# Performance work log

Hardware: AMD Instinct MI355X
Metric: run time of the kernel (lower is better)

Reference implementation:

```python
import jax, jax.numpy as jnp
import numpy as np
import math

NUM_HEADS = 8
EMBED = 512
D_K = EMBED // NUM_HEADS
B, T1, T2 = 16, 512, 512
N_POS = 2 * T1 - 1


def rel_shift(x, left_context=0):
    # x: (B, H, T1, 2*T1-1) -> (B, H, T1, T2), out[i, j] = x[i, j - i + T1 - 1]
    t1 = x.shape[2]
    t2 = t1 + left_context
    idx = jnp.arange(t2)[None, :] - jnp.arange(t1)[:, None] + (t1 - 1)  # (T1, T2)
    return jnp.take_along_axis(x, idx[None, None, :, :], axis=-1)


def setup_inputs() -> dict:
    key = jax.random.key(0)
    ks = jax.random.split(key, 16)
    scale = 1.0 / math.sqrt(EMBED)
    inp = {
        "query": jax.random.normal(ks[0], (B, T1, EMBED), jnp.float32),
        "key": jax.random.normal(ks[1], (B, T2, EMBED), jnp.float32),
        "value": jax.random.normal(ks[2], (B, T2, EMBED), jnp.float32),
        "pos_enc": jax.random.normal(ks[3], (B, N_POS, EMBED), jnp.float32),
        "mask": jnp.zeros((B, T2), dtype=bool),
        "chunk_mask": jnp.zeros((T1, T1), dtype=bool),
        "Wq": jax.random.normal(ks[4], (EMBED, EMBED), jnp.float32) * scale,
        "bq": jnp.zeros((EMBED,), jnp.float32),
        "Wk": jax.random.normal(ks[5], (EMBED, EMBED), jnp.float32) * scale,
        "bk": jnp.zeros((EMBED,), jnp.float32),
        "Wv": jax.random.normal(ks[6], (EMBED, EMBED), jnp.float32) * scale,
        "bv": jnp.zeros((EMBED,), jnp.float32),
        "Wpos": jax.random.normal(ks[7], (EMBED, EMBED), jnp.float32) * scale,
        "Wo": jax.random.normal(ks[8], (EMBED, EMBED), jnp.float32) * scale,
        "bo": jnp.zeros((EMBED,), jnp.float32),
        "pos_bias_u": jax.random.normal(ks[9], (NUM_HEADS, D_K), jnp.float32) * 0.1,
        "pos_bias_v": jax.random.normal(ks[10], (NUM_HEADS, D_K), jnp.float32) * 0.1,
        "left_context": 0,
    }
    return inp


def reference(query, key, value, pos_enc, mask, chunk_mask, Wq, bq, Wk, bk, Wv, bv,
              Wpos, Wo, bo, pos_bias_u, pos_bias_v, left_context):
    b, t1, _ = query.shape
    t2 = key.shape[1]
    # qkv projections -> (B, T, H, d_k)
    q = (query @ Wq.T + bq).reshape(b, t1, NUM_HEADS, D_K)
    k = (key @ Wk.T + bk).reshape(b, t2, NUM_HEADS, D_K)
    v = (value @ Wv.T + bv).reshape(b, t2, NUM_HEADS, D_K)
    # positional projection (no bias) -> (B, N, H, d_k)
    p = (pos_enc @ Wpos.T).reshape(b, -1, NUM_HEADS, D_K)
    # content and positional scores
    matrix_ac = jnp.einsum('bihd,bjhd->bhij', q + pos_bias_u, k)  # (B,H,T1,T2)
    matrix_bd = jnp.einsum('bihd,bnhd->bhin', q + pos_bias_v, p)  # (B,H,T1,N)
    matrix_bd = rel_shift(matrix_bd, left_context=left_context)   # (B,H,T1,T2)
    scores = (matrix_ac + matrix_bd) / math.sqrt(D_K)
    # combined mask: True = masked
    m = chunk_mask[None, None, :, :] | mask[:, None, None, :]
    neg_inf = jnp.finfo(scores.dtype).min
    scores = jnp.where(m, neg_inf, scores)
    attn = jax.nn.softmax(scores, axis=-1)
    attn = jnp.where(m, 0.0, attn)
    out = jnp.einsum('bhij,bjhd->bihd', attn, v).reshape(b, t1, NUM_HEADS * D_K)
    return out @ Wo.T + bo
```

## Files before the change

kernel.cpp:

```cpp
#include <hip/hip_runtime.h>
#include <math.h>

typedef _Float16 f16;
typedef f16 f16x8 __attribute__((ext_vector_type(8)));
typedef f16 f16x4 __attribute__((ext_vector_type(4)));
typedef float f32x4 __attribute__((ext_vector_type(4)));

#define H_   8
#define E_   512
#define DK   64
#define NPOS 1023

#define GLL(SRC, DST) __builtin_amdgcn_global_load_lds( \
    (const __attribute__((address_space(1))) void*)(SRC), \
    (__attribute__((address_space(3))) void*)(DST), 16, 0, 0)

struct CSeg { const float* src; f16* dst; int n4; };
struct CArgs { CSeg s[9]; };
__global__ __launch_bounds__(256) void conv_f16(CArgs a) {
    const int stride = gridDim.x * 256;
    const int gid = blockIdx.x * 256 + threadIdx.x;
    for (int si = 0; si < 9; ++si) {
        const float* __restrict__ src = a.s[si].src;
        f16* __restrict__ dst = a.s[si].dst;
        const int n4 = a.s[si].n4;
        for (int i = gid; i < n4; i += stride) {
            const float4 v = ((const float4*)src)[i];
            f16x4 h; h[0] = (f16)v.x; h[1] = (f16)v.y; h[2] = (f16)v.z; h[3] = (f16)v.w;
            ((f16x4*)dst)[i] = h;
        }
    }
}

struct PArg {
    const f16* A; const f16* W; const float* bias; const float* bias2;
    void* C; int Mvalid; int mode;
};
struct PArgs { PArg g[4]; };

__device__ __forceinline__ void gemm128_body(const PArg g, int bx, int by) {
    __shared__ __align__(16) f16 Al[128 * 32];
    __shared__ __align__(16) f16 Wl[128 * 32];
    const int tid = threadIdx.x;
    const int lane = tid & 63, w = tid >> 6;
    const int quad = lane >> 4, l15 = lane & 15;
    const int wr = w >> 1, wc = w & 1;
    const int m0 = by * 128, n0 = bx * 128;

    const int r0 = w * 32 + (lane >> 2);
    const int c0 = (lane & 3) * 8;
    int ar0 = m0 + r0;      if (ar0 >= g.Mvalid) ar0 = g.Mvalid - 1;
    int ar1 = m0 + r0 + 16; if (ar1 >= g.Mvalid) ar1 = g.Mvalid - 1;
    const f16* A0 = g.A + (size_t)ar0 * 512 + c0;
    const f16* A1 = g.A + (size_t)ar1 * 512 + c0;
    const f16* W0 = g.W + (size_t)(n0 + r0) * 512 + c0;
    const f16* W1 = g.W + (size_t)(n0 + r0 + 16) * 512 + c0;
    f16* const lA0 = &Al[(w * 32) * 32];
    f16* const lA1 = &Al[(w * 32 + 16) * 32];
    f16* const lW0 = &Wl[(w * 32) * 32];
    f16* const lW1 = &Wl[(w * 32 + 16) * 32];

    f32x4 acc[4][4];
    #pragma unroll
    for (int m = 0; m < 4; ++m)
        #pragma unroll
        for (int n = 0; n < 4; ++n) acc[m][n] = (f32x4){0.f, 0.f, 0.f, 0.f};

    for (int ki = 0; ki < 16; ++ki) {
        const int k0 = ki * 32;
        if (ki) __syncthreads();
        GLL(A0 + k0, lA0);
        GLL(A1 + k0, lA1);
        GLL(W0 + k0, lW0);
        GLL(W1 + k0, lW1);
        __syncthreads();

        f16x8 af[4], bf[4];
        #pragma unroll
        for (int m = 0; m < 4; ++m)
            af[m] = *(const f16x8*)&Al[(wr * 64 + m * 16 + l15) * 32 + quad * 8];
        #pragma unroll
        for (int n = 0; n < 4; ++n)
            bf[n] = *(const f16x8*)&Wl[(wc * 64 + n * 16 + l15) * 32 + quad * 8];
        #pragma unroll
        for (int m = 0; m < 4; ++m)
            #pragma unroll
            for (int n = 0; n < 4; ++n)
                acc[m][n] = __builtin_amdgcn_mfma_f32_16x16x32_f16(af[m], bf[n], acc[m][n], 0, 0, 0);
    }

    const int mq = m0 + wr * 64 + quad * 4;
    const int nq = n0 + wc * 64 + l15;
    #pragma unroll
    for (int m = 0; m < 4; ++m) {
        #pragma unroll
        for (int n = 0; n < 4; ++n) {
            const int gr0 = mq + m * 16;
            const int col = nq + n * 16;
            float bs = g.bias ? g.bias[col] : 0.f;
            if (g.bias2) bs += g.bias2[col];
            const f32x4 a = acc[m][n];
            if (g.mode == 0) {
                float* C = (float*)g.C;
                #pragma unroll
                for (int r = 0; r < 4; ++r) C[(size_t)(gr0 + r) * 512 + col] = a[r] + bs;
            } else if (g.mode == 1) {
                f16* C = (f16*)g.C;
                const int b = gr0 >> 9, t = gr0 & 511;
                const int hh = col >> 6, dk = col & 63;
                f16x4 hv;
                #pragma unroll
                for (int r = 0; r < 4; ++r) hv[r] = (f16)(a[r] + bs);
                *(f16x4*)&C[(((size_t)b * H_ + hh) * DK + dk) * 512 + t] = hv;
            } else if (g.mode == 2) {
                f16* C = (f16*)g.C;
                const int b = gr0 >> 9, t = gr0 & 511;
                const int hh = col >> 6, dk = col & 63;
                #pragma unroll
                for (int r = 0; r < 4; ++r)
                    C[(((size_t)b * H_ + hh) * 512 + t + r) * DK + dk] = (f16)(a[r] + bs);
            } else {
                f16* C = (f16*)g.C;
                const int hh = col >> 6, dk = col & 63;
                #pragma unroll
                for (int r = 0; r < 4; ++r) {
                    const int gm = gr0 + r;
                    if (gm < g.Mvalid) {
                        const int b = gm / NPOS, t = gm - b * NPOS;
                        C[(((size_t)b * H_ + hh) * NPOS + t) * DK + dk] = (f16)a[r];
                    }
                }
            }
        }
    }
}

__global__ __launch_bounds__(256, 4) void proj_all(PArgs a) {
    const int id = blockIdx.x;
    int gi, rem, nwg;
    if (id < 768) { gi = id >> 8; rem = id & 255; nwg = 256; }
    else          { gi = 3;       rem = id - 768; nwg = 512; }
    const int t = (rem & 7) * (nwg >> 3) + (rem >> 3);
    gemm128_body(a.g[gi], t & 3, t >> 2);
}
__global__ __launch_bounds__(256, 4) void proj_one(PArg g) {
    const int t = (blockIdx.x & 7) * 32 + (blockIdx.x >> 3);
    gemm128_body(g, t & 3, t >> 2);
}

__global__ __launch_bounds__(256) void attn_mfma(
    const f16* __restrict__ Qh,
    const f16* __restrict__ Kh,
    const f16* __restrict__ Vt,
    const f16* __restrict__ Ph,
    const float* __restrict__ pbu, const float* __restrict__ pbv,
    const unsigned char* __restrict__ bmask,
    const unsigned char* __restrict__ cmask,
    f16* __restrict__ CTX)
{
    __shared__ f16 Qa[64 * 72];
    __shared__ f16 Ka[64 * 72];
    __shared__ f16 Va[64 * 72];
    __shared__ f16 Pa[128 * 72];
    __shared__ unsigned char Ma[64 * 64];

    const int tid = threadIdx.x;
    const int lane = tid & 63, w = tid >> 6;
    const int quad = lane >> 4, l15 = lane & 15;
    const int id = blockIdx.x;
    const int lg = (id & 7) * 128 + (id >> 3);
    const int it = lg & 7, bh = lg >> 3;
    const int h = bh & 7, b = bh >> 3;
    const int i0 = it * 64;
    const int rowt = w * 16 + quad * 4;
    const int sr = tid >> 3, sc = (tid & 7) * 8;
    const int mr = tid >> 2, mc = (tid & 3) * 16;

    *(uint4*)&Qa[sr * 72 + sc] = *(const uint4*)&Qh[((size_t)bh * 512 + i0 + sr) * 64 + sc];
    *(uint4*)&Qa[(sr + 32) * 72 + sc] =
        *(const uint4*)&Qh[((size_t)bh * 512 + i0 + sr + 32) * 64 + sc];
    f16x8 dpbf[2];
    #pragma unroll
    for (int ks = 0; ks < 2; ++ks)
        #pragma unroll
        for (int j = 0; j < 8; ++j) {
            const int d = ks * 32 + quad * 8 + j;
            dpbf[ks][j] = (f16)(pbv[h * 64 + d] - pbu[h * 64 + d]);
        }

    float m_run[4], l_run[4];
    f32x4 accO[4];
    #pragma unroll
    for (int x = 0; x < 4; ++x) {
        m_run[x] = -__builtin_inff(); l_run[x] = 0.f;
        accO[x] = (f32x4){0.f, 0.f, 0.f, 0.f};
    }

    uint4 pK0, pK1, pV0, pV1, pP0, pP1, pP2, pP3, pM;
    {
        const int j0 = 0, nbase = 448 - i0;
        pK0 = *(const uint4*)&Kh[((size_t)bh * 512 + j0 + sr) * 64 + sc];
        pK1 = *(const uint4*)&Kh[((size_t)bh * 512 + j0 + sr + 32) * 64 + sc];
        pV0 = *(const uint4*)&Vt[((size_t)bh * 64 + sr) * 512 + j0 + sc];
        pV1 = *(const uint4*)&Vt[((size_t)bh * 64 + sr + 32) * 512 + j0 + sc];
        int n0_ = nbase + sr;       if (n0_ > NPOS - 1) n0_ = NPOS - 1;
        int n1_ = nbase + sr + 32;  if (n1_ > NPOS - 1) n1_ = NPOS - 1;
        int n2_ = nbase + sr + 64;  if (n2_ > NPOS - 1) n2_ = NPOS - 1;
        int n3_ = nbase + sr + 96;  if (n3_ > NPOS - 1) n3_ = NPOS - 1;
        pP0 = *(const uint4*)&Ph[((size_t)bh * NPOS + n0_) * 64 + sc];
        pP1 = *(const uint4*)&Ph[((size_t)bh * NPOS + n1_) * 64 + sc];
        pP2 = *(const uint4*)&Ph[((size_t)bh * NPOS + n2_) * 64 + sc];
        pP3 = *(const uint4*)&Ph[((size_t)bh * NPOS + n3_) * 64 + sc];
        const uint4 cm = *(const uint4*)&cmask[(size_t)(i0 + mr) * 512 + j0 + mc];
        const uint4 bm = *(const uint4*)&bmask[(size_t)b * 512 + j0 + mc];
        pM.x = cm.x | bm.x; pM.y = cm.y | bm.y; pM.z = cm.z | bm.z; pM.w = cm.w | bm.w;
    }

    for (int jt = 0; jt < 8; ++jt) {
        __syncthreads();
        *(uint4*)&Ka[sr * 72 + sc] = pK0;
        *(uint4*)&Ka[(sr + 32) * 72 + sc] = pK1;
        *(uint4*)&Va[sr * 72 + sc] = pV0;
        *(uint4*)&Va[(sr + 32) * 72 + sc] = pV1;
        *(uint4*)&Pa[sr * 72 + sc] = pP0;
        *(uint4*)&Pa[(sr + 32) * 72 + sc] = pP1;
        *(uint4*)&Pa[(sr + 64) * 72 + sc] = pP2;
        *(uint4*)&Pa[(sr + 96) * 72 + sc] = pP3;
        *(uint4*)&Ma[mr * 64 + mc] = pM;
        __syncthreads();

        if (jt < 7) {
            const int j0n = (jt + 1) * 64;
            const int nbase = j0n - i0 + 448;
            pK0 = *(const uint4*)&Kh[((size_t)bh * 512 + j0n + sr) * 64 + sc];
            pK1 = *(const uint4*)&Kh[((size_t)bh * 512 + j0n + sr + 32) * 64 + sc];
            pV0 = *(const uint4*)&Vt[((size_t)bh * 64 + sr) * 512 + j0n + sc];
            pV1 = *(const uint4*)&Vt[((size_t)bh * 64 + sr + 32) * 512 + j0n + sc];
            int n0_ = nbase + sr;       if (n0_ > NPOS - 1) n0_ = NPOS - 1;
            int n1_ = nbase + sr + 32;  if (n1_ > NPOS - 1) n1_ = NPOS - 1;
            int n2_ = nbase + sr + 64;  if (n2_ > NPOS - 1) n2_ = NPOS - 1;
            int n3_ = nbase + sr + 96;  if (n3_ > NPOS - 1) n3_ = NPOS - 1;
            pP0 = *(const uint4*)&Ph[((size_t)bh * NPOS + n0_) * 64 + sc];
            pP1 = *(const uint4*)&Ph[((size_t)bh * NPOS + n1_) * 64 + sc];
            pP2 = *(const uint4*)&Ph[((size_t)bh * NPOS + n2_) * 64 + sc];
            pP3 = *(const uint4*)&Ph[((size_t)bh * NPOS + n3_) * 64 + sc];
            const uint4 cm = *(const uint4*)&cmask[(size_t)(i0 + mr) * 512 + j0n + mc];
            const uint4 bm = *(const uint4*)&bmask[(size_t)b * 512 + j0n + mc];
            pM.x = cm.x | bm.x; pM.y = cm.y | bm.y; pM.z = cm.z | bm.z; pM.w = cm.w | bm.w;
        }

        f16x8 afQ[2], afV[2];
        #pragma unroll
        for (int ks = 0; ks < 2; ++ks) {
            afQ[ks] = *(const f16x8*)&Qa[(w * 16 + l15) * 72 + ks * 32 + quad * 8];
            afV[ks] = afQ[ks] + dpbf[ks];
        }
        f32x4 accAC[4];
        #pragma unroll
        for (int nt = 0; nt < 4; ++nt) {
            accAC[nt] = (f32x4){0.f, 0.f, 0.f, 0.f};
            #pragma unroll
            for (int ks = 0; ks < 2; ++ks) {
                const f16x8 bf = *(const f16x8*)&Ka[(nt * 16 + l15) * 72 + ks * 32 + quad * 8];
                accAC[nt] = __builtin_amdgcn_mfma_f32_16x16x32_f16(afQ[ks], bf, accAC[nt], 0, 0, 0);
            }
        }
        f32x4 accBD[5];
        #pragma unroll
        for (int u = 0; u < 5; ++u) {
            accBD[u] = (f32x4){0.f, 0.f, 0.f, 0.f};
            const int nts = (3 - w) + u;
            #pragma unroll
            for (int ks = 0; ks < 2; ++ks) {
                const f16x8 bf = *(const f16x8*)&Pa[(nts * 16 + l15) * 72 + ks * 32 + quad * 8];
                accBD[u] = __builtin_amdgcn_mfma_f32_16x16x32_f16(afV[ks], bf, accBD[u], 0, 0, 0);
            }
        }
        __syncthreads();

        #pragma unroll
        for (int rg = 0; rg < 4; ++rg) {
            const int qr = quad * 4 + rg;
            const int rt = rowt + rg;
            float tmpv[5];
            #pragma unroll
            for (int u = 0; u < 5; ++u) {
                const int cl = l15 + (3 + u) * 16 + qr - 63;
                const int dst = (quad * 16 + (cl & 15)) << 2;
                tmpv[u] = __uint_as_float(
                    (unsigned)__builtin_amdgcn_ds_permute(dst, (int)__float_as_uint(accBD[u][rg])));
            }
            const bool hi = l15 > qr;
            float sv[4]; unsigned mk = 0;
            #pragma unroll
            for (int nt = 0; nt < 4; ++nt) {
                const int c = nt * 16 + l15;
                const float bdv = hi ? tmpv[nt + 1] : tmpv[nt];
                float s = (accAC[nt][rg] + bdv) * 0.125f;
                if (Ma[rt * 64 + c]) { s = -3.402823466e38f; mk |= 1u << nt; }
                sv[nt] = s;
            }
            float tmax = fmaxf(fmaxf(sv[0], sv[1]), fmaxf(sv[2], sv[3]));
            #pragma unroll
            for (int d = 1; d < 16; d <<= 1) tmax = fmaxf(tmax, __shfl_xor(tmax, d));
            const float mnew = fmaxf(m_run[rg], tmax);
            const float alpha = __expf(m_run[rg] - mnew);
            float rsum = 0.f;
            f16 wv[4];
            #pragma unroll
            for (int nt = 0; nt < 4; ++nt) {
                const float e = __expf(sv[nt] - mnew);
                rsum += e;
                wv[nt] = ((mk >> nt) & 1u) ? (f16)0.f : (f16)e;
            }
            #pragma unroll
            for (int d = 1; d < 16; d <<= 1) rsum += __shfl_xor(rsum, d);
            l_run[rg] = l_run[rg] * alpha + rsum;
            m_run[rg] = mnew;
            #pragma unroll
            for (int dt = 0; dt < 4; ++dt) accO[dt][rg] *= alpha;
            #pragma unroll
            for (int nt = 0; nt < 4; ++nt)
                Ka[rt * 72 + nt * 16 + l15] = wv[nt];
        }
        f16x8 afW[2];
        #pragma unroll
        for (int ks = 0; ks < 2; ++ks)
            afW[ks] = *(const f16x8*)&Ka[(w * 16 + l15) * 72 + ks * 32 + quad * 8];
        #pragma unroll
        for (int dt = 0; dt < 4; ++dt)
            #pragma unroll
            for (int ks = 0; ks < 2; ++ks) {
                const f16x8 bf = *(const f16x8*)&Va[(dt * 16 + l15) * 72 + ks * 32 + quad * 8];
                accO[dt] = __builtin_amdgcn_mfma_f32_16x16x32_f16(afW[ks], bf, accO[dt], 0, 0, 0);
            }
    }

    #pragma unroll
    for (int rg = 0; rg < 4; ++rg) {
        const float inv = 1.0f / l_run[rg];
        const int gi = i0 + rowt + rg;
        #pragma unroll
        for (int dt = 0; dt < 4; ++dt)
            CTX[((size_t)b * 512 + gi) * 512 + h * 64 + dt * 16 + l15] = (f16)(accO[dt][rg] * inv);
    }
}

extern "C" void kernel_launch(void* const* d_in, const int* in_sizes, int n_in,
                              void* d_out, int out_size, void* d_ws, size_t ws_size,
                              hipStream_t stream) {
    const float* query   = (const float*)d_in[0];
    const float* key     = (const float*)d_in[1];
    const float* value   = (const float*)d_in[2];
    const float* pos_enc = (const float*)d_in[3];
    const unsigned char* mask       = (const unsigned char*)d_in[4];
    const unsigned char* chunk_mask = (const unsigned char*)d_in[5];
    const float* Wq  = (const float*)d_in[6];
    const float* bq  = (const float*)d_in[7];
    const float* Wk  = (const float*)d_in[8];
    const float* bk  = (const float*)d_in[9];
    const float* Wv  = (const float*)d_in[10];
    const float* bv  = (const float*)d_in[11];
    const float* Wpos = (const float*)d_in[12];
    const float* Wo   = (const float*)d_in[13];
    const float* bo   = (const float*)d_in[14];
    const float* pbu  = (const float*)d_in[15];
    const float* pbv  = (const float*)d_in[16];
    float* out = (float*)d_out;

    f16* base = (f16*)d_ws;
    size_t off = 0;
    f16* ctx  = base + off; off += 4194304;
    f16* Qhm  = base + off; off += 4194304;
    f16* Khm  = base + off; off += 4194304;
    f16* Vtm  = base + off; off += 4194304;
    f16* Phm  = base + off; off += 8380416;
    f16* qf   = base + off; off += 4194304;
    f16* kf   = base + off; off += 4194304;
    f16* vf   = base + off; off += 4194304;
    f16* pf   = base + off; off += 8380416;
    f16* wqf  = base + off; off += 262144;
    f16* wkf  = base + off; off += 262144;
    f16* wvf  = base + off; off += 262144;
    f16* wpf  = base + off; off += 262144;
    f16* wof  = base + off; off += 262144;

    CArgs ca;
    ca.s[0] = CSeg{pos_enc, pf,  2095104};
    ca.s[1] = CSeg{query,   qf,  1048576};
    ca.s[2] = CSeg{key,     kf,  1048576};
    ca.s[3] = CSeg{value,   vf,  1048576};
    ca.s[4] = CSeg{Wq,      wqf, 65536};
    ca.s[5] = CSeg{Wk,      wkf, 65536};
    ca.s[6] = CSeg{Wv,      wvf, 65536};
    ca.s[7] = CSeg{Wpos,    wpf, 65536};
    ca.s[8] = CSeg{Wo,      wof, 65536};
    conv_f16<<<dim3(2048), 256, 0, stream>>>(ca);

    PArgs pa;
    pa.g[0] = PArg{qf, wqf, bq, pbu,     (void*)Qhm, 8192,  2};
    pa.g[1] = PArg{kf, wkf, bk, nullptr, (void*)Khm, 8192,  2};
    pa.g[2] = PArg{vf, wvf, bv, nullptr, (void*)Vtm, 8192,  1};
    pa.g[3] = PArg{pf, wpf, nullptr, nullptr, (void*)Phm, 16368, 3};
    proj_all<<<dim3(1280), 256, 0, stream>>>(pa);

    attn_mfma<<<dim3(1024), 256, 0, stream>>>(Qhm, Khm, Vtm, Phm, pbu, pbv,
                                              mask, chunk_mask, ctx);

    PArg go = PArg{ctx, wof, bo, nullptr, (void*)out, 8192, 0};
    proj_one<<<dim3(256), 256, 0, stream>>>(go);
}
```

Baseline: 270.3 us.

## Fold softmax scale into Q projection and keep Q fragments in registers

The 1/sqrt(d_k) scale moves into the Q projection epilogue and the pos-bias difference term, so the per-score multiply in the attention loop goes away. Q fragments are loaded straight from global into registers once, instead of being staged through an LDS buffer and re-read every KV iteration, which frees LDS. The attention kernel also gets a launch_bounds occupancy hint of 4 blocks. Pre-scaling Q before the fp16 rounding changes rounding slightly, and the occupancy hint may cap registers and cause spills.

Measured after the change: 282.7 us. 4.6% more time.

```diff
diff --git a/kernel.cpp b/kernel.cpp
--- a/kernel.cpp
+++ b/kernel.cpp
@@ -34,7 +34,7 @@
 
 struct PArg {
     const f16* A; const f16* W; const float* bias; const float* bias2;
-    void* C; int Mvalid; int mode;
+    void* C; int Mvalid; int mode; float scale;
 };
 struct PArgs { PArg g[4]; };
 
@@ -110,7 +110,7 @@
                 const int hh = col >> 6, dk = col & 63;
                 f16x4 hv;
                 #pragma unroll
-                for (int r = 0; r < 4; ++r) hv[r] = (f16)(a[r] + bs);
+                for (int r = 0; r < 4; ++r) hv[r] = (f16)((a[r] + bs) * g.scale);
                 *(f16x4*)&C[(((size_t)b * H_ + hh) * DK + dk) * 512 + t] = hv;
             } else if (g.mode == 2) {
                 f16* C = (f16*)g.C;
@@ -118,7 +118,7 @@
                 const int hh = col >> 6, dk = col & 63;
                 #pragma unroll
                 for (int r = 0; r < 4; ++r)
-                    C[(((size_t)b * H_ + hh) * 512 + t + r) * DK + dk] = (f16)(a[r] + bs);
+                    C[(((size_t)b * H_ + hh) * 512 + t + r) * DK + dk] = (f16)((a[r] + bs) * g.scale);
             } else {
                 f16* C = (f16*)g.C;
                 const int hh = col >> 6, dk = col & 63;
@@ -148,7 +148,7 @@
     gemm128_body(g, t & 3, t >> 2);
 }
 
-__global__ __launch_bounds__(256) void attn_mfma(
+__global__ __launch_bounds__(256, 4) void attn_mfma(
     const f16* __restrict__ Qh,
     const f16* __restrict__ Kh,
     const f16* __restrict__ Vt,
@@ -158,7 +158,6 @@
     const unsigned char* __restrict__ cmask,
     f16* __restrict__ CTX)
 {
-    __shared__ f16 Qa[64 * 72];
     __shared__ f16 Ka[64 * 72];
     __shared__ f16 Va[64 * 72];
     __shared__ f16 Pa[128 * 72];
@@ -176,17 +175,22 @@
     const int sr = tid >> 3, sc = (tid & 7) * 8;
     const int mr = tid >> 2, mc = (tid & 3) * 16;
 
-    *(uint4*)&Qa[sr * 72 + sc] = *(const uint4*)&Qh[((size_t)bh * 512 + i0 + sr) * 64 + sc];
-    *(uint4*)&Qa[(sr + 32) * 72 + sc] =
-        *(const uint4*)&Qh[((size_t)bh * 512 + i0 + sr + 32) * 64 + sc];
-    f16x8 dpbf[2];
-    #pragma unroll
-    for (int ks = 0; ks < 2; ++ks)
-        #pragma unroll
-        for (int j = 0; j < 8; ++j) {
-            const int d = ks * 32 + quad * 8 + j;
-            dpbf[ks][j] = (f16)(pbv[h * 64 + d] - pbu[h * 64 + d]);
-        }
+    f16x8 afQ[2], afV[2];
+    {
+        const f16* qp = &Qh[((size_t)bh * 512 + i0 + w * 16 + l15) * 64 + quad * 8];
+        afQ[0] = *(const f16x8*)qp;
+        afQ[1] = *(const f16x8*)(qp + 32);
+        #pragma unroll
+        for (int ks = 0; ks < 2; ++ks) {
+            f16x8 d;
+            #pragma unroll
+            for (int j = 0; j < 8; ++j) {
+                const int dd = ks * 32 + quad * 8 + j;
+                d[j] = (f16)(0.125f * (pbv[h * 64 + dd] - pbu[h * 64 + dd]));
+            }
+            afV[ks] = afQ[ks] + d;
+        }
+    }
 
     float m_run[4], l_run[4];
     f32x4 accO[4];
@@ -249,12 +253,6 @@
             pM.x = cm.x | bm.x; pM.y = cm.y | bm.y; pM.z = cm.z | bm.z; pM.w = cm.w | bm.w;
         }
 
-        f16x8 afQ[2], afV[2];
-        #pragma unroll
-        for (int ks = 0; ks < 2; ++ks) {
-            afQ[ks] = *(const f16x8*)&Qa[(w * 16 + l15) * 72 + ks * 32 + quad * 8];
-            afV[ks] = afQ[ks] + dpbf[ks];
-        }
         f32x4 accAC[4];
         #pragma unroll
         for (int nt = 0; nt < 4; ++nt) {
@@ -296,7 +294,7 @@
             for (int nt = 0; nt < 4; ++nt) {
                 const int c = nt * 16 + l15;
                 const float bdv = hi ? tmpv[nt + 1] : tmpv[nt];
-                float s = (accAC[nt][rg] + bdv) * 0.125f;
+                float s = accAC[nt][rg] + bdv;
                 if (Ma[rt * 64 + c]) { s = -3.402823466e38f; mk |= 1u << nt; }
                 sv[nt] = s;
             }
@@ -398,15 +396,15 @@
     conv_f16<<<dim3(2048), 256, 0, stream>>>(ca);
 
     PArgs pa;
-    pa.g[0] = PArg{qf, wqf, bq, pbu,     (void*)Qhm, 8192,  2};
-    pa.g[1] = PArg{kf, wkf, bk, nullptr, (void*)Khm, 8192,  2};
-    pa.g[2] = PArg{vf, wvf, bv, nullptr, (void*)Vtm, 8192,  1};
-    pa.g[3] = PArg{pf, wpf, nullptr, nullptr, (void*)Phm, 16368, 3};
+    pa.g[0] = PArg{qf, wqf, bq, pbu,     (void*)Qhm, 8192,  2, 0.125f};
+    pa.g[1] = PArg{kf, wkf, bk, nullptr, (void*)Khm, 8192,  2, 1.0f};
+    pa.g[2] = PArg{vf, wvf, bv, nullptr, (void*)Vtm, 8192,  1, 1.0f};
+    pa.g[3] = PArg{pf, wpf, nullptr, nullptr, (void*)Phm, 16368, 3, 1.0f};
     proj_all<<<dim3(1280), 256, 0, stream>>>(pa);
 
     attn_mfma<<<dim3(1024), 256, 0, stream>>>(Qhm, Khm, Vtm, Phm, pbu, pbv,
                                               mask, chunk_mask, ctx);
 
-    PArg go = PArg{ctx, wof, bo, nullptr, (void*)out, 8192, 0};
+    PArg go = PArg{ctx, wof, bo, nullptr, (void*)out, 8192, 0, 1.0f};
     proj_one<<<dim3(256), 256, 0, stream>>>(go);
 }
```
